# Optimization experiments

Measured on AMD Instinct MI355X. Metric: run time of the kernel, lower is better.

## Reference

```python
import jax, jax.numpy as jnp
import numpy as np

N_NODES = 50000
N_EDGES = 800000
D_IN = 128
D_OUT = 128


def setup_inputs() -> dict:
    key = jax.random.key(0)
    ks = jax.random.split(key, 6)
    x = jax.random.normal(ks[0], (N_NODES, D_IN), dtype=jnp.float32)
    edge_src = jax.random.randint(ks[1], (N_EDGES,), 0, N_NODES)
    edge_dst = jax.random.randint(ks[2], (N_EDGES,), 0, N_NODES)
    edge_val = jax.random.uniform(ks[3], (N_EDGES,), dtype=jnp.float32)
    W = jax.random.normal(ks[4], (D_OUT, D_IN), dtype=jnp.float32) / np.sqrt(D_IN)
    b = jax.random.normal(ks[5], (D_OUT,), dtype=jnp.float32) * 0.01
    return {"x": x, "edge_src": edge_src, "edge_dst": edge_dst,
            "edge_val": edge_val, "W": W, "b": b}


def reference(x, edge_src, edge_dst, edge_val, W, b):
    # h = sparse.mm(adj, x): for each edge (dst, src, val): h[dst] += val * x[src]
    msgs = edge_val[:, None] * x[edge_src]            # [E, D_IN]
    h = jax.ops.segment_sum(msgs, edge_dst, num_segments=N_NODES)  # [N, D_IN]
    # nn.Linear: h @ W.T + b, then relu activation
    out = jnp.einsum('nd,od->no', h, W) + b           # [N, D_OUT]
    return jax.nn.relu(out)
```

## Files before the change

### kernel.cpp

```cpp
#include <hip/hip_runtime.h>
#include <hip/hip_bf16.h>

#define N_NODES 50000
#define N_EDGES 800000
#define D 128
#define SCAN_NB 49

static_assert(N_NODES < 65536, "src must fit in 16 bits for epack");

typedef __attribute__((ext_vector_type(8))) short short8;
typedef __attribute__((ext_vector_type(4))) float f32x4;
typedef unsigned int uint;
typedef unsigned short ushort;

__device__ __forceinline__ ushort f2bf(float f) {
    uint u = __float_as_uint(f);
    u += 0x7fffu + ((u >> 16) & 1u);
    return (ushort)(u >> 16);
}

__device__ __forceinline__ float bflo(uint u) { return __uint_as_float(u << 16); }
__device__ __forceinline__ float bfhi(uint u) { return __uint_as_float(u & 0xffff0000u); }


__global__ __launch_bounds__(256) void sgcn_prep(
    const float* __restrict__ W, ushort* __restrict__ Wb, int* __restrict__ deg)
{
    int t = blockIdx.x * 256 + threadIdx.x;
    if (t < (D * D) / 4) {
        float4 a = reinterpret_cast<const float4*>(W)[t];
        ushort4 s;
        s.x = f2bf(a.x); s.y = f2bf(a.y); s.z = f2bf(a.z); s.w = f2bf(a.w);
        *reinterpret_cast<ushort4*>(Wb + (size_t)t * 4) = s;
    }
    if (t < N_NODES / 4) {
        reinterpret_cast<int4*>(deg)[t] = make_int4(0, 0, 0, 0);
    }
}


__global__ __launch_bounds__(256) void sgcn_hist_rank(
    const int* __restrict__ dst, int* __restrict__ deg, int* __restrict__ rank)
{
    int e = blockIdx.x * 256 + threadIdx.x;
    if (e < N_EDGES)
        rank[e] = atomicAdd(&deg[dst[e]], 1);
}

__global__ __launch_bounds__(256) void sgcn_scanf(
    const int* __restrict__ deg, int* __restrict__ rowptr)
{
    __shared__ int part[256];
    __shared__ int soff;
    int tid = threadIdx.x;
    int b = blockIdx.x;

    const int4* d4 = reinterpret_cast<const int4*>(deg);
    int pre = 0;
    for (int i = tid; i < b * 256; i += 256) {
        int4 v = d4[i];
        pre += v.x + v.y + v.z + v.w;
    }
    part[tid] = pre;
    __syncthreads();
    for (int off = 128; off > 0; off >>= 1) {
        if (tid < off) part[tid] += part[tid + off];
        __syncthreads();
    }
    if (tid == 0) soff = part[0];
    __syncthreads();

    int base = b * 1024 + tid * 4;
    int4 v = make_int4(0, 0, 0, 0);
    if (base < N_NODES) v = *reinterpret_cast<const int4*>(deg + base);
    int s = v.x + v.y + v.z + v.w;
    part[tid] = s;
    __syncthreads();
    for (int off = 1; off < 256; off <<= 1) {
        int mine  = part[tid];
        int other = (tid >= off) ? part[tid - off] : 0;
        __syncthreads();
        part[tid] = mine + other;
        __syncthreads();
    }
    int run = soff + ((tid == 0) ? 0 : part[tid - 1]);
    if (base < N_NODES) {
        int4 r;
        r.x = run;
        r.y = run + v.x;
        r.z = r.y + v.y;
        r.w = r.z + v.z;
        *reinterpret_cast<int4*>(rowptr + base) = r;
        if (base + 4 == N_NODES) rowptr[N_NODES] = r.w + v.w;
    }
}

__global__ __launch_bounds__(256) void sgcn_permute(
    const int* __restrict__ src, const int* __restrict__ dst,
    const float* __restrict__ val, const int* __restrict__ rowptr,
    const int* __restrict__ rank, uint* __restrict__ epack)
{
    int e = blockIdx.x * 256 + threadIdx.x;
    if (e < N_EDGES) {
        int pos = rowptr[dst[e]] + rank[e];
        epack[pos] = ((uint)f2bf(val[e]) << 16) | (uint)src[e];
    }
}


__global__ __launch_bounds__(256) void sgcn_gemm_y(
    const float* __restrict__ x, const ushort* __restrict__ Wb,
    ushort* __restrict__ y)
{
    int wave = threadIdx.x >> 6;
    int lane = threadIdx.x & 63;
    int lm = lane & 15;
    int kb = lane >> 4;

    short8 bfr[8][4];
#pragma unroll
    for (int nt = 0; nt < 8; ++nt)
#pragma unroll
        for (int kk = 0; kk < 4; ++kk)
            bfr[nt][kk] = *reinterpret_cast<const short8*>(
                Wb + (nt * 16 + lm) * D + kk * 32 + kb * 8);

    const int nMT = N_NODES / 16;
    int mt0 = blockIdx.x * 4 + wave;
    int strideMT = gridDim.x * 4;
    for (int mt = mt0; mt < nMT; mt += strideMT) {
        int m0 = mt * 16;
        const float* xrow = x + (long)(m0 + lm) * D + kb * 8;
        short8 afr[4];
#pragma unroll
        for (int kk = 0; kk < 4; ++kk) {
            float4 a = *reinterpret_cast<const float4*>(xrow + kk * 32);
            float4 c = *reinterpret_cast<const float4*>(xrow + kk * 32 + 4);
            short8 s;
            s[0] = (short)f2bf(a.x); s[1] = (short)f2bf(a.y);
            s[2] = (short)f2bf(a.z); s[3] = (short)f2bf(a.w);
            s[4] = (short)f2bf(c.x); s[5] = (short)f2bf(c.y);
            s[6] = (short)f2bf(c.z); s[7] = (short)f2bf(c.w);
            afr[kk] = s;
        }
#pragma unroll
        for (int nt = 0; nt < 8; ++nt) {
            f32x4 acc = {0.f, 0.f, 0.f, 0.f};
#pragma unroll
            for (int kk = 0; kk < 4; ++kk)
                acc = __builtin_amdgcn_mfma_f32_16x16x32_bf16(afr[kk], bfr[nt][kk], acc, 0, 0, 0);
            ushort* yp = y + (long)(m0 + kb * 4) * D + nt * 16 + lm;
#pragma unroll
            for (int r = 0; r < 4; ++r)
                yp[(long)r * D] = f2bf(acc[r]);
        }
    }
}


__global__ __launch_bounds__(256) void sgcn_aggregate(
    const uint* __restrict__ yb, const int* __restrict__ rowptr,
    const uint* __restrict__ ep, const float* __restrict__ bias,
    float* __restrict__ out)
{
    int gw   = (blockIdx.x * 256 + threadIdx.x) >> 6;
    int lane = threadIdx.x & 63;
    int q    = lane >> 4;
    int c    = lane & 15;
    int nW   = (gridDim.x * 256) >> 6;
    float4 bv0 = *reinterpret_cast<const float4*>(bias + c * 8);
    float4 bv1 = *reinterpret_cast<const float4*>(bias + c * 8 + 4);

    for (int n = gw; n < N_NODES; n += nW) {
        int j0 = rowptr[n], j1 = rowptr[n + 1];
        float a0 = 0.f, a1 = 0.f, a2 = 0.f, a3 = 0.f;
        float a4 = 0.f, a5 = 0.f, a6 = 0.f, a7 = 0.f;
        int j = j0;
        for (; j + 8 <= j1; j += 8) {
            uint p0 = ep[j + q];
            uint p1 = ep[j + 4 + q];
            uint4 u0 = *reinterpret_cast<const uint4*>(yb + (size_t)(p0 & 0xffffu) * 64 + c * 4);
            uint4 u1 = *reinterpret_cast<const uint4*>(yb + (size_t)(p1 & 0xffffu) * 64 + c * 4);
            float v0 = __uint_as_float(p0 & 0xffff0000u);
            float v1 = __uint_as_float(p1 & 0xffff0000u);
            a0 += v0 * bflo(u0.x) + v1 * bflo(u1.x);
            a1 += v0 * bfhi(u0.x) + v1 * bfhi(u1.x);
            a2 += v0 * bflo(u0.y) + v1 * bflo(u1.y);
            a3 += v0 * bfhi(u0.y) + v1 * bfhi(u1.y);
            a4 += v0 * bflo(u0.z) + v1 * bflo(u1.z);
            a5 += v0 * bfhi(u0.z) + v1 * bfhi(u1.z);
            a6 += v0 * bflo(u0.w) + v1 * bflo(u1.w);
            a7 += v0 * bfhi(u0.w) + v1 * bfhi(u1.w);
        }
        for (; j < j1; j += 4) {
            int jj = j + q;
            if (jj < j1) {
                uint p = ep[jj];
                uint4 u = *reinterpret_cast<const uint4*>(yb + (size_t)(p & 0xffffu) * 64 + c * 4);
                float v = __uint_as_float(p & 0xffff0000u);
                a0 += v * bflo(u.x); a1 += v * bfhi(u.x);
                a2 += v * bflo(u.y); a3 += v * bfhi(u.y);
                a4 += v * bflo(u.z); a5 += v * bfhi(u.z);
                a6 += v * bflo(u.w); a7 += v * bfhi(u.w);
            }
        }
        a0 += __shfl_xor(a0, 16); a0 += __shfl_xor(a0, 32);
        a1 += __shfl_xor(a1, 16); a1 += __shfl_xor(a1, 32);
        a2 += __shfl_xor(a2, 16); a2 += __shfl_xor(a2, 32);
        a3 += __shfl_xor(a3, 16); a3 += __shfl_xor(a3, 32);
        a4 += __shfl_xor(a4, 16); a4 += __shfl_xor(a4, 32);
        a5 += __shfl_xor(a5, 16); a5 += __shfl_xor(a5, 32);
        a6 += __shfl_xor(a6, 16); a6 += __shfl_xor(a6, 32);
        a7 += __shfl_xor(a7, 16); a7 += __shfl_xor(a7, 32);
        if (q == 0) {
            f32x4 r0, r1;
            r0[0] = fmaxf(a0 + bv0.x, 0.f);
            r0[1] = fmaxf(a1 + bv0.y, 0.f);
            r0[2] = fmaxf(a2 + bv0.z, 0.f);
            r0[3] = fmaxf(a3 + bv0.w, 0.f);
            r1[0] = fmaxf(a4 + bv1.x, 0.f);
            r1[1] = fmaxf(a5 + bv1.y, 0.f);
            r1[2] = fmaxf(a6 + bv1.z, 0.f);
            r1[3] = fmaxf(a7 + bv1.w, 0.f);
            f32x4* op = reinterpret_cast<f32x4*>(out + (long)n * D + c * 8);
            __builtin_nontemporal_store(r0, op);
            __builtin_nontemporal_store(r1, op + 1);
        }
    }
}

extern "C" void kernel_launch(void* const* d_in, const int* in_sizes, int n_in,
                              void* d_out, int out_size, void* d_ws, size_t ws_size,
                              hipStream_t stream) {
    const float* x   = (const float*)d_in[0];
    const int*   es  = (const int*)d_in[1];
    const int*   ed  = (const int*)d_in[2];
    const float* ev  = (const float*)d_in[3];
    const float* W   = (const float*)d_in[4];
    const float* b   = (const float*)d_in[5];
    float* out = (float*)d_out;

    char* ws = (char*)d_ws;
    size_t off = 0;
    uint*   yb       = (uint*)  (ws + off); off += (size_t)N_NODES * (D / 2) * sizeof(uint);
    ushort* Wb       = (ushort*)(ws + off); off += (size_t)D * D * sizeof(ushort);
    uint*   epack    = (uint*)  (ws + off); off += (size_t)N_EDGES * sizeof(uint);
    int*    rowptr   = (int*)   (ws + off); off += ((size_t)(N_NODES + 1) * sizeof(int) + 15) & ~15ull;
    int*    deg      = (int*)   (ws + off); off += (size_t)N_NODES * sizeof(int);
    int* rank = (int*)d_out;

    const int EB = (N_EDGES + 255) / 256;

    sgcn_prep<<<64, 256, 0, stream>>>(W, Wb, deg);
    sgcn_gemm_y<<<512, 256, 0, stream>>>(x, Wb, (ushort*)yb);
    sgcn_hist_rank<<<EB, 256, 0, stream>>>(ed, deg, rank);
    sgcn_scanf<<<SCAN_NB, 256, 0, stream>>>(deg, rowptr);
    sgcn_permute<<<EB, 256, 0, stream>>>(es, ed, ev, rowptr, rank, epack);
    sgcn_aggregate<<<2048, 256, 0, stream>>>(yb, rowptr, epack, b, out);
}
```

Baseline: 116.2 us.

## Fuse CSR build into cooperative kernel and use 16-lane-per-node aggregation

Merges the histogram/rank, scan and permute kernels into one cooperative-launch kernel separated by grid-wide syncs, with the old three-kernel path kept as a fallback if the cooperative launch fails. This is meant to remove two kernel launch gaps. Separately, the aggregate kernel now gives each node 16 lanes with no grid-stride loop, unrolls 4 edges per iteration and drops the cross-quarter shuffle reduction. The cost is longer serial per-node loops, with more outstanding gathers per lane. Grid syncs add their own overhead.

```diff
diff --git a/kernel.cpp b/kernel.cpp
--- a/kernel.cpp
+++ b/kernel.cpp
@@ -1,5 +1,8 @@
 #include <hip/hip_runtime.h>
 #include <hip/hip_bf16.h>
+#include <hip/hip_cooperative_groups.h>
+
+namespace cg = cooperative_groups;
 
 #define N_NODES 50000
 #define N_EDGES 800000
@@ -39,22 +42,10 @@
 }
 
 
-__global__ __launch_bounds__(256) void sgcn_hist_rank(
-    const int* __restrict__ dst, int* __restrict__ deg, int* __restrict__ rank)
-{
-    int e = blockIdx.x * 256 + threadIdx.x;
-    if (e < N_EDGES)
-        rank[e] = atomicAdd(&deg[dst[e]], 1);
-}
-
-__global__ __launch_bounds__(256) void sgcn_scanf(
-    const int* __restrict__ deg, int* __restrict__ rowptr)
-{
-    __shared__ int part[256];
-    __shared__ int soff;
-    int tid = threadIdx.x;
-    int b = blockIdx.x;
-
+__device__ __forceinline__ void scan_block_body(
+    const int* __restrict__ deg, int* __restrict__ rowptr, int b, int tid,
+    int* part , int* soff )
+{
     const int4* d4 = reinterpret_cast<const int4*>(deg);
     int pre = 0;
     for (int i = tid; i < b * 256; i += 256) {
@@ -67,7 +58,7 @@
         if (tid < off) part[tid] += part[tid + off];
         __syncthreads();
     }
-    if (tid == 0) soff = part[0];
+    if (tid == 0) *soff = part[0];
     __syncthreads();
 
     int base = b * 1024 + tid * 4;
@@ -83,7 +74,7 @@
         part[tid] = mine + other;
         __syncthreads();
     }
-    int run = soff + ((tid == 0) ? 0 : part[tid - 1]);
+    int run = *soff + ((tid == 0) ? 0 : part[tid - 1]);
     if (base < N_NODES) {
         int4 r;
         r.x = run;
@@ -93,6 +84,49 @@
         *reinterpret_cast<int4*>(rowptr + base) = r;
         if (base + 4 == N_NODES) rowptr[N_NODES] = r.w + v.w;
     }
+}
+
+
+__global__ __launch_bounds__(256) void sgcn_csr(
+    const int* __restrict__ src, const int* __restrict__ dst,
+    const float* __restrict__ val, int* __restrict__ deg,
+    int* __restrict__ rank, int* __restrict__ rowptr, uint* __restrict__ epack)
+{
+    cg::grid_group grid = cg::this_grid();
+    __shared__ int part[256];
+    __shared__ int soff;
+    int tid = blockIdx.x * 256 + threadIdx.x;
+    int stride = gridDim.x * 256;
+
+    for (int e = tid; e < N_EDGES; e += stride)
+        rank[e] = atomicAdd(&deg[dst[e]], 1);
+    grid.sync();
+
+    if (blockIdx.x < SCAN_NB)
+        scan_block_body(deg, rowptr, blockIdx.x, threadIdx.x, part, &soff);
+    grid.sync();
+
+    for (int e = tid; e < N_EDGES; e += stride) {
+        int pos = rowptr[dst[e]] + rank[e];
+        epack[pos] = ((uint)f2bf(val[e]) << 16) | (uint)src[e];
+    }
+}
+
+
+__global__ __launch_bounds__(256) void sgcn_hist_rank(
+    const int* __restrict__ dst, int* __restrict__ deg, int* __restrict__ rank)
+{
+    int e = blockIdx.x * 256 + threadIdx.x;
+    if (e < N_EDGES)
+        rank[e] = atomicAdd(&deg[dst[e]], 1);
+}
+
+__global__ __launch_bounds__(256) void sgcn_scanf(
+    const int* __restrict__ deg, int* __restrict__ rowptr)
+{
+    __shared__ int part[256];
+    __shared__ int soff;
+    scan_block_body(deg, rowptr, blockIdx.x, threadIdx.x, part, &soff);
 }
 
 __global__ __launch_bounds__(256) void sgcn_permute(
@@ -163,70 +197,55 @@
     const uint* __restrict__ ep, const float* __restrict__ bias,
     float* __restrict__ out)
 {
-    int gw   = (blockIdx.x * 256 + threadIdx.x) >> 6;
-    int lane = threadIdx.x & 63;
-    int q    = lane >> 4;
-    int c    = lane & 15;
-    int nW   = (gridDim.x * 256) >> 6;
+    int n = (blockIdx.x * 256 + threadIdx.x) >> 4;
+    int c = threadIdx.x & 15;
     float4 bv0 = *reinterpret_cast<const float4*>(bias + c * 8);
     float4 bv1 = *reinterpret_cast<const float4*>(bias + c * 8 + 4);
 
-    for (int n = gw; n < N_NODES; n += nW) {
-        int j0 = rowptr[n], j1 = rowptr[n + 1];
-        float a0 = 0.f, a1 = 0.f, a2 = 0.f, a3 = 0.f;
-        float a4 = 0.f, a5 = 0.f, a6 = 0.f, a7 = 0.f;
-        int j = j0;
-        for (; j + 8 <= j1; j += 8) {
-            uint p0 = ep[j + q];
-            uint p1 = ep[j + 4 + q];
-            uint4 u0 = *reinterpret_cast<const uint4*>(yb + (size_t)(p0 & 0xffffu) * 64 + c * 4);
-            uint4 u1 = *reinterpret_cast<const uint4*>(yb + (size_t)(p1 & 0xffffu) * 64 + c * 4);
-            float v0 = __uint_as_float(p0 & 0xffff0000u);
-            float v1 = __uint_as_float(p1 & 0xffff0000u);
-            a0 += v0 * bflo(u0.x) + v1 * bflo(u1.x);
-            a1 += v0 * bfhi(u0.x) + v1 * bfhi(u1.x);
-            a2 += v0 * bflo(u0.y) + v1 * bflo(u1.y);
-            a3 += v0 * bfhi(u0.y) + v1 * bfhi(u1.y);
-            a4 += v0 * bflo(u0.z) + v1 * bflo(u1.z);
-            a5 += v0 * bfhi(u0.z) + v1 * bfhi(u1.z);
-            a6 += v0 * bflo(u0.w) + v1 * bflo(u1.w);
-            a7 += v0 * bfhi(u0.w) + v1 * bfhi(u1.w);
-        }
-        for (; j < j1; j += 4) {
-            int jj = j + q;
-            if (jj < j1) {
-                uint p = ep[jj];
-                uint4 u = *reinterpret_cast<const uint4*>(yb + (size_t)(p & 0xffffu) * 64 + c * 4);
-                float v = __uint_as_float(p & 0xffff0000u);
-                a0 += v * bflo(u.x); a1 += v * bfhi(u.x);
-                a2 += v * bflo(u.y); a3 += v * bfhi(u.y);
-                a4 += v * bflo(u.z); a5 += v * bfhi(u.z);
-                a6 += v * bflo(u.w); a7 += v * bfhi(u.w);
-            }
-        }
-        a0 += __shfl_xor(a0, 16); a0 += __shfl_xor(a0, 32);
-        a1 += __shfl_xor(a1, 16); a1 += __shfl_xor(a1, 32);
-        a2 += __shfl_xor(a2, 16); a2 += __shfl_xor(a2, 32);
-        a3 += __shfl_xor(a3, 16); a3 += __shfl_xor(a3, 32);
-        a4 += __shfl_xor(a4, 16); a4 += __shfl_xor(a4, 32);
-        a5 += __shfl_xor(a5, 16); a5 += __shfl_xor(a5, 32);
-        a6 += __shfl_xor(a6, 16); a6 += __shfl_xor(a6, 32);
-        a7 += __shfl_xor(a7, 16); a7 += __shfl_xor(a7, 32);
-        if (q == 0) {
-            f32x4 r0, r1;
-            r0[0] = fmaxf(a0 + bv0.x, 0.f);
-            r0[1] = fmaxf(a1 + bv0.y, 0.f);
-            r0[2] = fmaxf(a2 + bv0.z, 0.f);
-            r0[3] = fmaxf(a3 + bv0.w, 0.f);
-            r1[0] = fmaxf(a4 + bv1.x, 0.f);
-            r1[1] = fmaxf(a5 + bv1.y, 0.f);
-            r1[2] = fmaxf(a6 + bv1.z, 0.f);
-            r1[3] = fmaxf(a7 + bv1.w, 0.f);
-            f32x4* op = reinterpret_cast<f32x4*>(out + (long)n * D + c * 8);
-            __builtin_nontemporal_store(r0, op);
-            __builtin_nontemporal_store(r1, op + 1);
-        }
-    }
+    int j0 = rowptr[n], j1 = rowptr[n + 1];
+    float a0 = 0.f, a1 = 0.f, a2 = 0.f, a3 = 0.f;
+    float a4 = 0.f, a5 = 0.f, a6 = 0.f, a7 = 0.f;
+    int j = j0;
+    for (; j + 4 <= j1; j += 4) {
+        uint p0 = ep[j], p1 = ep[j + 1], p2 = ep[j + 2], p3 = ep[j + 3];
+        uint4 u0 = *reinterpret_cast<const uint4*>(yb + (size_t)(p0 & 0xffffu) * 64 + c * 4);
+        uint4 u1 = *reinterpret_cast<const uint4*>(yb + (size_t)(p1 & 0xffffu) * 64 + c * 4);
+        uint4 u2 = *reinterpret_cast<const uint4*>(yb + (size_t)(p2 & 0xffffu) * 64 + c * 4);
+        uint4 u3 = *reinterpret_cast<const uint4*>(yb + (size_t)(p3 & 0xffffu) * 64 + c * 4);
+        float v0 = __uint_as_float(p0 & 0xffff0000u);
+        float v1 = __uint_as_float(p1 & 0xffff0000u);
+        float v2 = __uint_as_float(p2 & 0xffff0000u);
+        float v3 = __uint_as_float(p3 & 0xffff0000u);
+        a0 += v0 * bflo(u0.x) + v1 * bflo(u1.x) + v2 * bflo(u2.x) + v3 * bflo(u3.x);
+        a1 += v0 * bfhi(u0.x) + v1 * bfhi(u1.x) + v2 * bfhi(u2.x) + v3 * bfhi(u3.x);
+        a2 += v0 * bflo(u0.y) + v1 * bflo(u1.y) + v2 * bflo(u2.y) + v3 * bflo(u3.y);
+        a3 += v0 * bfhi(u0.y) + v1 * bfhi(u1.y) + v2 * bfhi(u2.y) + v3 * bfhi(u3.y);
+        a4 += v0 * bflo(u0.z) + v1 * bflo(u1.z) + v2 * bflo(u2.z) + v3 * bflo(u3.z);
+        a5 += v0 * bfhi(u0.z) + v1 * bfhi(u1.z) + v2 * bfhi(u2.z) + v3 * bfhi(u3.z);
+        a6 += v0 * bflo(u0.w) + v1 * bflo(u1.w) + v2 * bflo(u2.w) + v3 * bflo(u3.w);
+        a7 += v0 * bfhi(u0.w) + v1 * bfhi(u1.w) + v2 * bfhi(u2.w) + v3 * bfhi(u3.w);
+    }
+    for (; j < j1; ++j) {
+        uint p = ep[j];
+        uint4 u = *reinterpret_cast<const uint4*>(yb + (size_t)(p & 0xffffu) * 64 + c * 4);
+        float v = __uint_as_float(p & 0xffff0000u);
+        a0 += v * bflo(u.x); a1 += v * bfhi(u.x);
+        a2 += v * bflo(u.y); a3 += v * bfhi(u.y);
+        a4 += v * bflo(u.z); a5 += v * bfhi(u.z);
+        a6 += v * bflo(u.w); a7 += v * bfhi(u.w);
+    }
+    f32x4 r0, r1;
+    r0[0] = fmaxf(a0 + bv0.x, 0.f);
+    r0[1] = fmaxf(a1 + bv0.y, 0.f);
+    r0[2] = fmaxf(a2 + bv0.z, 0.f);
+    r0[3] = fmaxf(a3 + bv0.w, 0.f);
+    r1[0] = fmaxf(a4 + bv1.x, 0.f);
+    r1[1] = fmaxf(a5 + bv1.y, 0.f);
+    r1[2] = fmaxf(a6 + bv1.z, 0.f);
+    r1[3] = fmaxf(a7 + bv1.w, 0.f);
+    f32x4* op = reinterpret_cast<f32x4*>(out + (long)n * D + c * 8);
+    __builtin_nontemporal_store(r0, op);
+    __builtin_nontemporal_store(r1, op + 1);
 }
 
 extern "C" void kernel_launch(void* const* d_in, const int* in_sizes, int n_in,
@@ -242,19 +261,30 @@
 
     char* ws = (char*)d_ws;
     size_t off = 0;
-    uint*   yb       = (uint*)  (ws + off); off += (size_t)N_NODES * (D / 2) * sizeof(uint);
-    ushort* Wb       = (ushort*)(ws + off); off += (size_t)D * D * sizeof(ushort);
-    uint*   epack    = (uint*)  (ws + off); off += (size_t)N_EDGES * sizeof(uint);
-    int*    rowptr   = (int*)   (ws + off); off += ((size_t)(N_NODES + 1) * sizeof(int) + 15) & ~15ull;
-    int*    deg      = (int*)   (ws + off); off += (size_t)N_NODES * sizeof(int);
+    uint*   yb     = (uint*)  (ws + off); off += (size_t)N_NODES * (D / 2) * sizeof(uint);
+    ushort* Wb     = (ushort*)(ws + off); off += (size_t)D * D * sizeof(ushort);
+    uint*   epack  = (uint*)  (ws + off); off += (size_t)N_EDGES * sizeof(uint);
+    int*    rowptr = (int*)   (ws + off); off += ((size_t)(N_NODES + 1) * sizeof(int) + 15) & ~15ull;
+    int*    deg    = (int*)   (ws + off); off += (size_t)N_NODES * sizeof(int);
     int* rank = (int*)d_out;
 
     const int EB = (N_EDGES + 255) / 256;
 
     sgcn_prep<<<64, 256, 0, stream>>>(W, Wb, deg);
     sgcn_gemm_y<<<512, 256, 0, stream>>>(x, Wb, (ushort*)yb);
-    sgcn_hist_rank<<<EB, 256, 0, stream>>>(ed, deg, rank);
-    sgcn_scanf<<<SCAN_NB, 256, 0, stream>>>(deg, rowptr);
-    sgcn_permute<<<EB, 256, 0, stream>>>(es, ed, ev, rowptr, rank, epack);
-    sgcn_aggregate<<<2048, 256, 0, stream>>>(yb, rowptr, epack, b, out);
-}
+
+    {
+        const int* src_ = es; const int* dst_ = ed; const float* val_ = ev;
+        int* deg_ = deg; int* rank_ = rank; int* rowptr_ = rowptr; uint* epack_ = epack;
+        void* args[] = {&src_, &dst_, &val_, &deg_, &rank_, &rowptr_, &epack_};
+        hipError_t cerr = hipLaunchCooperativeKernel(
+            (const void*)sgcn_csr, dim3(1024), dim3(256), args, 0, stream);
+        if (cerr != hipSuccess) {
+            sgcn_hist_rank<<<EB, 256, 0, stream>>>(ed, deg, rank);
+            sgcn_scanf<<<SCAN_NB, 256, 0, stream>>>(deg, rowptr);
+            sgcn_permute<<<EB, 256, 0, stream>>>(es, ed, ev, rowptr, rank, epack);
+        }
+    }
+
+    sgcn_aggregate<<<3125, 256, 0, stream>>>(yb, rowptr, epack, b, out);
+}
```

After: 309.3 us. 166% more time.
